# Kernel tuning notes

Hardware: AMD Instinct MI355X
Metric: run time of the kernel (lower is better)

Reference implementation:

```python
import jax, jax.numpy as jnp
import numpy as np


def setup_inputs() -> dict:
    key = jax.random.key(0)
    kq, kk, kv = jax.random.split(key, 3)
    B, L, S, H, E, D = 2, 2048, 2048, 16, 64, 64
    return {
        "queries": jax.random.normal(kq, (B, L, H, E), dtype=jnp.float32),
        "keys": jax.random.normal(kk, (B, S, H, E), dtype=jnp.float32),
        "values": jax.random.normal(kv, (B, S, H, D), dtype=jnp.float32),
    }


def reference(queries, keys, values):
    # FullAttention forward (mask_flag=False, dropout=0.0 -> identity)
    E = queries.shape[-1]
    scale = 1.0 / jnp.sqrt(jnp.asarray(E, dtype=queries.dtype))
    # scores: [B, H, L, S]
    scores = jnp.einsum('blhe,bshe->bhls', queries, keys)
    A = jax.nn.softmax(scale * scores, axis=-1)
    # output: [B, L, H, D]
    V = jnp.einsum('bhls,bshd->blhd', A, values)
    return V
```

## Files before the change

### kernel.cpp

```cpp
#include <hip/hip_runtime.h>
#include <hip/hip_bf16.h>
#include <string.h>


#define NB 2
#define LL 2048
#define SS 2048
#define HH 16
#define EE 64
#define DD 64
#define KVB 64
#define NT (SS / KVB)
#define NWG2 (NB * HH * (LL / 64))

typedef _Float16 f16x8 __attribute__((ext_vector_type(8)));
typedef float f32x4 __attribute__((ext_vector_type(4)));
typedef float f32x16 __attribute__((ext_vector_type(16)));
typedef unsigned uint2v __attribute__((ext_vector_type(2)));
typedef unsigned uint4v __attribute__((ext_vector_type(4)));
typedef const __attribute__((address_space(1))) void* gas_p;
typedef __attribute__((address_space(3))) void* las_p;

__device__ __forceinline__ unsigned pk2h(float a, float b) {
    auto h = __builtin_amdgcn_cvt_pkrtz(a, b);
    unsigned u;
    __builtin_memcpy(&u, &h, 4);
    return u;
}

__device__ __forceinline__ float fexp2(float x) {
#if defined(__has_builtin) && __has_builtin(__builtin_amdgcn_exp2f)
    return __builtin_amdgcn_exp2f(x);
#else
    return exp2f(x);
#endif
}

__device__ __forceinline__ void gll16(const void* g, void* l) {
    __builtin_amdgcn_global_load_lds((gas_p)g, (las_p)l, 16, 0, 0);
}

__device__ __forceinline__ uint2v plswap(unsigned a, unsigned b) {
#if defined(__has_builtin) && __has_builtin(__builtin_amdgcn_permlane32_swap)
    return __builtin_amdgcn_permlane32_swap(a, b, false, false);
#else
    unsigned ax = (unsigned)__shfl_xor((int)a, 32);
    unsigned bx = (unsigned)__shfl_xor((int)b, 32);
    int l32 = (int)(threadIdx.x & 32);
    uint2v r;
    r[0] = l32 ? bx : a;
    r[1] = l32 ? b : ax;
    return r;
#endif
}

__device__ __forceinline__ float fbits(unsigned u) {
    float f; __builtin_memcpy(&f, &u, 4); return f;
}
__device__ __forceinline__ unsigned ubits(float f) {
    unsigned u; __builtin_memcpy(&u, &f, 4); return u;
}
__device__ __forceinline__ float xmax32(float x) {
    uint2v r = plswap(ubits(x), ubits(x));
    return fmaxf(fbits(r[0]), fbits(r[1]));
}
__device__ __forceinline__ float xsum32(float x) {
    uint2v r = plswap(ubits(x), ubits(x));
    return fbits(r[0]) + fbits(r[1]);
}

__global__ __launch_bounds__(256) void prepKV(const float* __restrict__ K,
                                              const float* __restrict__ V,
                                              unsigned short* __restrict__ Kh,
                                              unsigned short* __restrict__ Vth) {
    const int NTILE = NB * HH * NT;
    const bool isV = blockIdx.x >= NTILE;
    const int tile = blockIdx.x & (NTILE - 1);
    const int it = tile & (NT - 1);
    const int bh = tile >> 5;
    const int b = bh >> 4, h = bh & 15;
    const int t = threadIdx.x;

    if (!isV) {
        const int s = t >> 2, ec = t & 3;
        const float* src = K + (((size_t)b * SS + it * KVB + s) * HH + h) * EE + ec * 16;
        f32x4 x0 = ((const f32x4*)src)[0];
        f32x4 x1 = ((const f32x4*)src)[1];
        f32x4 x2 = ((const f32x4*)src)[2];
        f32x4 x3 = ((const f32x4*)src)[3];
        uint4v c0, c1;
        c0.x = pk2h(x0[0], x0[1]); c0.y = pk2h(x0[2], x0[3]);
        c0.z = pk2h(x1[0], x1[1]); c0.w = pk2h(x1[2], x1[3]);
        c1.x = pk2h(x2[0], x2[1]); c1.y = pk2h(x2[2], x2[3]);
        c1.z = pk2h(x3[0], x3[1]); c1.w = pk2h(x3[2], x3[3]);
        char* dst = (char*)Kh + (size_t)tile * 8192;
        const int sw = (s & 7) << 4;
        *(uint4v*)(dst + ((s * 128 + ec * 32) ^ sw)) = c0;
        *(uint4v*)(dst + ((s * 128 + ec * 32 + 16) ^ sw)) = c1;
    } else {
        __shared__ float Vt[64 * 68];
        {
            const int s = t >> 2, dc = t & 3;
            const float* src = V + (((size_t)b * SS + it * KVB + s) * HH + h) * DD + dc * 16;
            f32x4 x0 = ((const f32x4*)src)[0];
            f32x4 x1 = ((const f32x4*)src)[1];
            f32x4 x2 = ((const f32x4*)src)[2];
            f32x4 x3 = ((const f32x4*)src)[3];
            float* row = Vt + s * 68 + dc * 16;
            ((f32x4*)row)[0] = x0; ((f32x4*)row)[1] = x1;
            ((f32x4*)row)[2] = x2; ((f32x4*)row)[3] = x3;
        }
        __syncthreads();
        {
            const int d = t >> 2, sc = t & 3;
            float w[16];
#pragma unroll
            for (int j = 0; j < 16; ++j) w[j] = Vt[(sc * 16 + j) * 68 + d];
            uint4v c0, c1;
            c0.x = pk2h(w[0], w[1]); c0.y = pk2h(w[2], w[3]);
            c0.z = pk2h(w[4], w[5]); c0.w = pk2h(w[6], w[7]);
            c1.x = pk2h(w[8], w[9]); c1.y = pk2h(w[10], w[11]);
            c1.z = pk2h(w[12], w[13]); c1.w = pk2h(w[14], w[15]);
            char* dst = (char*)Vth + (size_t)tile * 8192;
            const int sw = (d & 7) << 4;
            *(uint4v*)(dst + ((d * 128 + sc * 32) ^ sw)) = c0;
            *(uint4v*)(dst + ((d * 128 + sc * 32 + 16) ^ sw)) = c1;
        }
    }
}

__global__ __launch_bounds__(256, 4) void fattn4(const unsigned short* __restrict__ Kh,
                                                 const unsigned short* __restrict__ Vth,
                                                 const float* __restrict__ Q,
                                                 float* __restrict__ O) {
    __shared__ __align__(16) char LB[32768];
    __shared__ float msh[4][32];
    __shared__ float lsh[4][32];
    char* K0s = LB;
    char* K1s = LB + 8192;
    char* V0s = LB + 16384;
    char* V1s = LB + 24576;

    const int tid = threadIdx.x;
    const int lane = tid & 63;
    const int wid = tid >> 6;
    const int ln = lane & 31;
    const int hi = lane >> 5;
    const int qg = wid >> 1;
    const int sh = wid & 1;

    const int bid0 = blockIdx.x;
    const int bid = (bid0 & 7) * (NWG2 >> 3) + (bid0 >> 3);
    const int bh = bid >> 5;
    const int qt = bid & 31;
    const int b = bh >> 4, h = bh & 15;
    const int qrow = qt * 64 + qg * 32 + ln;

    const float qs = 0.125f * 1.44269504088896340736f;
    const float* qptr = Q + (((size_t)b * LL + qrow) * HH + h) * EE + hi * 8;
    f16x8 qf[4];
#pragma unroll
    for (int ks = 0; ks < 4; ++ks) {
        f32x4 a0 = *(const f32x4*)(qptr + ks * 16);
        f32x4 a1 = *(const f32x4*)(qptr + ks * 16 + 4);
        union { f16x8 v; unsigned u[4]; } cv;
        cv.u[0] = pk2h(a0[0] * qs, a0[1] * qs);
        cv.u[1] = pk2h(a0[2] * qs, a0[3] * qs);
        cv.u[2] = pk2h(a1[0] * qs, a1[1] * qs);
        cv.u[3] = pk2h(a1[2] * qs, a1[3] * qs);
        qf[ks] = cv.v;
    }

    f32x16 o0, o1;
#pragma unroll
    for (int i = 0; i < 16; ++i) { o0[i] = 0.f; o1[i] = 0.f; }
    float m = -1e30f, l = 0.f;

    const char* Kg = (const char*)Kh + (size_t)bh * (NT * 8192);
    const char* Vg = (const char*)Vth + (size_t)bh * (NT * 8192);

    auto STAGE = [&](int it, char* Ks, char* Vs) {
        const size_t off = (size_t)it * 8192 + wid * 2048 + lane * 16;
        gll16(Kg + off, Ks + wid * 2048);
        gll16(Kg + off + 1024, Ks + wid * 2048 + 1024);
        gll16(Vg + off, Vs + wid * 2048);
        gll16(Vg + off + 1024, Vs + wid * 2048 + 1024);
    };

    const int swz = (ln & 7) << 4;
    const int srow = sh * 32 + ln;
    const int vcol = sh * 64;

    auto COMPUTE = [&](const char* Ks, const char* Vs) {
        f32x16 st;
#pragma unroll
        for (int i = 0; i < 16; ++i) st[i] = 0.f;
        __builtin_amdgcn_s_setprio(1);
#pragma unroll
        for (int ks = 0; ks < 4; ++ks) {
            f16x8 kf = *(const f16x8*)(Ks + ((srow * 128 + ks * 32 + hi * 16) ^ swz));
            st = __builtin_amdgcn_mfma_f32_32x32x16_f16(kf, qf[ks], st, 0, 0, 0);
        }
        __builtin_amdgcn_s_setprio(0);

        float x0 = st[0], x1 = st[1], x2 = st[2], x3 = st[3];
#pragma unroll
        for (int r = 4; r < 16; r += 4) {
            x0 = fmaxf(x0, st[r]);
            x1 = fmaxf(x1, st[r + 1]);
            x2 = fmaxf(x2, st[r + 2]);
            x3 = fmaxf(x3, st[r + 3]);
        }
        float pmax = xmax32(fmaxf(fmaxf(x0, x1), fmaxf(x2, x3)));
        if (!__all(pmax - m <= 8.0f)) {
            const float mn = fmaxf(m, pmax);
            const float al = fexp2(m - mn);
            l *= al; m = mn;
#pragma unroll
            for (int i = 0; i < 16; ++i) { o0[i] *= al; o1[i] *= al; }
        }
        float t0 = 0.f, t1 = 0.f, t2 = 0.f, t3 = 0.f;
#pragma unroll
        for (int r = 0; r < 16; r += 4) {
            st[r] = fexp2(st[r] - m);
            st[r + 1] = fexp2(st[r + 1] - m);
            st[r + 2] = fexp2(st[r + 2] - m);
            st[r + 3] = fexp2(st[r + 3] - m);
            t0 += st[r]; t1 += st[r + 1]; t2 += st[r + 2]; t3 += st[r + 3];
        }
        l += (t0 + t1) + (t2 + t3);

        {
            uint2v r0 = plswap(pk2h(st[0], st[1]), pk2h(st[4], st[5]));
            uint2v r1 = plswap(pk2h(st[2], st[3]), pk2h(st[6], st[7]));
            union { f16x8 v; unsigned u[4]; } w;
            w.u[0] = r0[0]; w.u[1] = r1[0]; w.u[2] = r0[1]; w.u[3] = r1[1];
            f16x8 v0 = *(const f16x8*)(Vs + ((ln * 128 + vcol + hi * 16) ^ swz));
            f16x8 v1 = *(const f16x8*)(Vs + (((32 + ln) * 128 + vcol + hi * 16) ^ swz));
            __builtin_amdgcn_s_setprio(1);
            o0 = __builtin_amdgcn_mfma_f32_32x32x16_f16(v0, w.v, o0, 0, 0, 0);
            o1 = __builtin_amdgcn_mfma_f32_32x32x16_f16(v1, w.v, o1, 0, 0, 0);
            __builtin_amdgcn_s_setprio(0);
        }
        {
            uint2v r2 = plswap(pk2h(st[8], st[9]), pk2h(st[12], st[13]));
            uint2v r3 = plswap(pk2h(st[10], st[11]), pk2h(st[14], st[15]));
            union { f16x8 v; unsigned u[4]; } w;
            w.u[0] = r2[0]; w.u[1] = r3[0]; w.u[2] = r2[1]; w.u[3] = r3[1];
            f16x8 v0 = *(const f16x8*)(Vs + ((ln * 128 + vcol + 32 + hi * 16) ^ swz));
            f16x8 v1 = *(const f16x8*)(Vs + (((32 + ln) * 128 + vcol + 32 + hi * 16) ^ swz));
            __builtin_amdgcn_s_setprio(1);
            o0 = __builtin_amdgcn_mfma_f32_32x32x16_f16(v0, w.v, o0, 0, 0, 0);
            o1 = __builtin_amdgcn_mfma_f32_32x32x16_f16(v1, w.v, o1, 0, 0, 0);
            __builtin_amdgcn_s_setprio(0);
        }
    };

    STAGE(0, K0s, V0s);
    __syncthreads();
    for (int it = 0; it < NT; it += 2) {
        if (it + 1 < NT) STAGE(it + 1, K1s, V1s);
        COMPUTE(K0s, V0s);
        __syncthreads();
        if (it + 2 < NT) STAGE(it + 2, K0s, V0s);
        COMPUTE(K1s, V1s);
        __syncthreads();
    }

    l = xsum32(l);
    if (hi == 0) { msh[wid][ln] = m; lsh[wid][ln] = l; }
    __syncthreads();
    const float mo = msh[wid ^ 1][ln];
    const float lo = lsh[wid ^ 1][ln];
    const float ms = fmaxf(m, mo);
    const float f = fexp2(m - ms);
    const float fo = fexp2(mo - ms);
    const float lstar = l * f + lo * fo;

    float* pbuf = (float*)LB + qg * (32 * 65);
    if (sh == 1) {
#pragma unroll
        for (int r = 0; r < 16; ++r) {
            const int d = (r & 3) + 8 * (r >> 2) + 4 * hi;
            pbuf[ln * 65 + d] = o0[r] * f;
            pbuf[ln * 65 + 32 + d] = o1[r] * f;
        }
    }
    __syncthreads();
    if (sh == 0) {
        const float invl = 1.f / lstar;
        float* optr = O + (((size_t)b * LL + qrow) * HH + h) * DD;
#pragma unroll
        for (int t = 0; t < 4; ++t) {
            f32x4 w0, w1;
#pragma unroll
            for (int i = 0; i < 4; ++i) {
                const int d = t * 8 + hi * 4 + i;
                w0[i] = (o0[4 * t + i] * f + pbuf[ln * 65 + d]) * invl;
                w1[i] = (o1[4 * t + i] * f + pbuf[ln * 65 + 32 + d]) * invl;
            }
            *(f32x4*)(optr + t * 8 + hi * 4) = w0;
            *(f32x4*)(optr + 32 + t * 8 + hi * 4) = w1;
        }
    }
}

typedef unsigned u2f __attribute__((ext_vector_type(2)));
__global__ __launch_bounds__(256) void fattn1(const float* __restrict__ Q,
                                              const float* __restrict__ K,
                                              const float* __restrict__ V,
                                              float* __restrict__ O) {
    __shared__ __align__(16) short Klds[KVB * 64];
    __shared__ __align__(16) short Vtlds[64 * KVB];
    __shared__ __align__(16) short Plds[4][16 * 64];

    const int tid = threadIdx.x;
    const int lane = tid & 63;
    const int wid = tid >> 6;
    const int g = (lane >> 4) & 3;
    const int c = lane & 15;

    const int bid = blockIdx.x;
    const int bh = bid >> 5;
    const int qt = bid & 31;
    const int b = bh >> 4;
    const int h = bh & 15;
    const int q0 = qt * 64;

    const int qrow = q0 + wid * 16 + c;
    const float* qptr = Q + (((size_t)b * LL + qrow) * HH + h) * EE;
    const float qs = 0.125f * 1.44269504088896340736f;
    f16x8 qf[2];
#pragma unroll
    for (int kk = 0; kk < 2; ++kk) {
        f32x4 a0 = *(const f32x4*)(qptr + kk * 32 + g * 8);
        f32x4 a1 = *(const f32x4*)(qptr + kk * 32 + g * 8 + 4);
        union { f16x8 v; unsigned u[4]; } cv;
        cv.u[0] = pk2h(a0[0] * qs, a0[1] * qs);
        cv.u[1] = pk2h(a0[2] * qs, a0[3] * qs);
        cv.u[2] = pk2h(a1[0] * qs, a1[1] * qs);
        cv.u[3] = pk2h(a1[2] * qs, a1[3] * qs);
        qf[kk] = cv.v;
    }

    f32x4 osacc[4];
    const f32x4 fzero = {0.f, 0.f, 0.f, 0.f};
#pragma unroll
    for (int i = 0; i < 4; ++i) osacc[i] = fzero;
    float m_run = -1e30f;
    float l_run = 0.f;

    const int km = tid & 15;
    const int kr = tid >> 4;

    for (int it = 0; it < NT; ++it) {
        const int s_glob = it * KVB;
        f32x4 kreg[4];
#pragma unroll
        for (int p = 0; p < 4; ++p) {
            int s = kr + p * 16;
            kreg[p] = *(const f32x4*)(K + (((size_t)b * SS + s_glob + s) * HH + h) * EE + km * 4);
        }
        f32x4 vreg[4];
#pragma unroll
        for (int p = 0; p < 4; ++p) {
            int s = kr * 4 + p;
            vreg[p] = *(const f32x4*)(V + (((size_t)b * SS + s_glob + s) * HH + h) * DD + km * 4);
        }
        __syncthreads();
#pragma unroll
        for (int p = 0; p < 4; ++p) {
            int s = kr + p * 16;
            u2f w;
            w.x = pk2h(kreg[p][0], kreg[p][1]);
            w.y = pk2h(kreg[p][2], kreg[p][3]);
            int byte = (s * 128 + km * 8) ^ ((s & 7) << 4);
            *(u2f*)((char*)Klds + byte) = w;
        }
#pragma unroll
        for (int i = 0; i < 4; ++i) {
            int d = km * 4 + i;
            u2f w;
            w.x = pk2h(vreg[0][i], vreg[1][i]);
            w.y = pk2h(vreg[2][i], vreg[3][i]);
            int byte = (d * 128 + kr * 8) ^ ((d & 7) << 4);
            *(u2f*)((char*)Vtlds + byte) = w;
        }
        __syncthreads();

        f32x4 stv[4];
#pragma unroll
        for (int fr = 0; fr < 4; ++fr) stv[fr] = fzero;
#pragma unroll
        for (int fr = 0; fr < 4; ++fr) {
            int s = fr * 16 + c;
            f16x8 kf0 = *(const f16x8*)((const char*)Klds + ((s * 128 + 16 * g) ^ ((s & 7) << 4)));
            stv[fr] = __builtin_amdgcn_mfma_f32_16x16x32_f16(kf0, qf[0], stv[fr], 0, 0, 0);
            f16x8 kf1 = *(const f16x8*)((const char*)Klds + ((s * 128 + 64 + 16 * g) ^ ((s & 7) << 4)));
            stv[fr] = __builtin_amdgcn_mfma_f32_16x16x32_f16(kf1, qf[1], stv[fr], 0, 0, 0);
        }

        float pmax = stv[0][0];
#pragma unroll
        for (int fr = 0; fr < 4; ++fr)
#pragma unroll
            for (int r = 0; r < 4; ++r) pmax = fmaxf(pmax, stv[fr][r]);
        pmax = fmaxf(pmax, __shfl_xor(pmax, 16));
        pmax = fmaxf(pmax, __shfl_xor(pmax, 32));
        float mnew = fmaxf(m_run, pmax);
        float alpha = fexp2(m_run - mnew);
        float tsum = 0.f;
#pragma unroll
        for (int fr = 0; fr < 4; ++fr)
#pragma unroll
            for (int r = 0; r < 4; ++r) {
                float e = fexp2(stv[fr][r] - mnew);
                stv[fr][r] = e;
                tsum += e;
            }
        tsum += __shfl_xor(tsum, 16);
        tsum += __shfl_xor(tsum, 32);
        l_run = l_run * alpha + tsum;
        m_run = mnew;
#pragma unroll
        for (int fr = 0; fr < 4; ++fr)
#pragma unroll
            for (int r = 0; r < 4; ++r) osacc[fr][r] *= alpha;

        short* plb = &Plds[wid][0];
#pragma unroll
        for (int fr = 0; fr < 4; ++fr) {
            u2f w;
            w.x = pk2h(stv[fr][0], stv[fr][1]);
            w.y = pk2h(stv[fr][2], stv[fr][3]);
            int byte = (c * 128 + fr * 32 + g * 8) ^ ((c & 7) << 4);
            *(u2f*)((char*)plb + byte) = w;
        }
        f16x8 pb0 = *(const f16x8*)((const char*)plb + ((c * 128 + 16 * g) ^ ((c & 7) << 4)));
        f16x8 pb1 = *(const f16x8*)((const char*)plb + ((c * 128 + 64 + 16 * g) ^ ((c & 7) << 4)));

#pragma unroll
        for (int fr = 0; fr < 4; ++fr) {
            int d = fr * 16 + c;
            f16x8 vf0 = *(const f16x8*)((const char*)Vtlds + ((d * 128 + 16 * g) ^ ((d & 7) << 4)));
            osacc[fr] = __builtin_amdgcn_mfma_f32_16x16x32_f16(vf0, pb0, osacc[fr], 0, 0, 0);
            f16x8 vf1 = *(const f16x8*)((const char*)Vtlds + ((d * 128 + 64 + 16 * g) ^ ((d & 7) << 4)));
            osacc[fr] = __builtin_amdgcn_mfma_f32_16x16x32_f16(vf1, pb1, osacc[fr], 0, 0, 0);
        }
    }

    float invl = 1.f / l_run;
    float* optr = O + (((size_t)b * LL + qrow) * HH + h) * DD;
#pragma unroll
    for (int fr = 0; fr < 4; ++fr) {
        f32x4 o;
        o[0] = osacc[fr][0] * invl;
        o[1] = osacc[fr][1] * invl;
        o[2] = osacc[fr][2] * invl;
        o[3] = osacc[fr][3] * invl;
        *(f32x4*)(optr + fr * 16 + g * 4) = o;
    }
}

extern "C" void kernel_launch(void* const* d_in, const int* in_sizes, int n_in,
                              void* d_out, int out_size, void* d_ws, size_t ws_size,
                              hipStream_t stream) {
    const float* Q = (const float*)d_in[0];
    const float* K = (const float*)d_in[1];
    const float* V = (const float*)d_in[2];
    float* Op = (float*)d_out;

    const size_t halfBytes = (size_t)NB * HH * SS * EE * 2;
    if (ws_size >= 2 * halfBytes) {
        unsigned short* Kht = (unsigned short*)d_ws;
        unsigned short* Vht = (unsigned short*)((char*)d_ws + halfBytes);
        hipLaunchKernelGGL(prepKV, dim3(2 * NB * HH * NT), dim3(256), 0, stream, K, V, Kht, Vht);
        hipLaunchKernelGGL(fattn4, dim3(NWG2), dim3(256), 0, stream, Kht, Vht, Q, Op);
    } else {
        hipLaunchKernelGGL(fattn1, dim3(NB * HH * (LL / 64)), dim3(256), 0, stream, Q, K, V, Op);
    }
}
```

Before: 67.48 us.

## Load V fragments directly from global and software-pipeline QK with softmax-PV

Stops staging V tiles through LDS: each lane now reads its V fragments straight from global memory into registers, and only K is double-buffered in LDS, which shrinks shared memory from about 33KB to about 18KB. The loop is restructured so the QK MFMA for the next tile is issued before the softmax and PV of the current tile, overlapping matrix work with exp and reduction work. The trade is uncoalesced global V loads with their latency exposed inside the loop, plus extra registers for a second score accumulator.

```diff
diff --git a/kernel.cpp b/kernel.cpp
--- a/kernel.cpp
+++ b/kernel.cpp
@@ -129,17 +129,11 @@
     }
 }
 
-__global__ __launch_bounds__(256, 4) void fattn4(const unsigned short* __restrict__ Kh,
+__global__ __launch_bounds__(256, 4) void fattn5(const unsigned short* __restrict__ Kh,
                                                  const unsigned short* __restrict__ Vth,
                                                  const float* __restrict__ Q,
                                                  float* __restrict__ O) {
-    __shared__ __align__(16) char LB[32768];
-    __shared__ float msh[4][32];
-    __shared__ float lsh[4][32];
-    char* K0s = LB;
-    char* K1s = LB + 8192;
-    char* V0s = LB + 16384;
-    char* V1s = LB + 24576;
+    __shared__ __align__(16) char LB[18176];
 
     const int tid = threadIdx.x;
     const int lane = tid & 63;
@@ -155,6 +149,9 @@
     const int qt = bid & 31;
     const int b = bh >> 4, h = bh & 15;
     const int qrow = qt * 64 + qg * 32 + ln;
+
+    char* KA = LB;
+    char* KB = LB + 8192;
 
     const float qs = 0.125f * 1.44269504088896340736f;
     const float* qptr = Q + (((size_t)b * LL + qrow) * HH + h) * EE + hi * 8;
@@ -179,20 +176,21 @@
     const char* Kg = (const char*)Kh + (size_t)bh * (NT * 8192);
     const char* Vg = (const char*)Vth + (size_t)bh * (NT * 8192);
 
-    auto STAGE = [&](int it, char* Ks, char* Vs) {
+    const int swz = (ln & 7) << 4;
+    const int srow = sh * 32 + ln;
+    const int vcol = sh * 64;
+    const int vo00 = (ln * 128 + vcol + hi * 16) ^ swz;
+    const int vo01 = ((32 + ln) * 128 + vcol + hi * 16) ^ swz;
+    const int vo10 = (ln * 128 + vcol + 32 + hi * 16) ^ swz;
+    const int vo11 = ((32 + ln) * 128 + vcol + 32 + hi * 16) ^ swz;
+
+    auto STAGE_K = [&](int it, char* Ks) {
         const size_t off = (size_t)it * 8192 + wid * 2048 + lane * 16;
         gll16(Kg + off, Ks + wid * 2048);
         gll16(Kg + off + 1024, Ks + wid * 2048 + 1024);
-        gll16(Vg + off, Vs + wid * 2048);
-        gll16(Vg + off + 1024, Vs + wid * 2048 + 1024);
     };
 
-    const int swz = (ln & 7) << 4;
-    const int srow = sh * 32 + ln;
-    const int vcol = sh * 64;
-
-    auto COMPUTE = [&](const char* Ks, const char* Vs) {
-        f32x16 st;
+    auto QK = [&](const char* Ks, f32x16& st) {
 #pragma unroll
         for (int i = 0; i < 16; ++i) st[i] = 0.f;
         __builtin_amdgcn_s_setprio(1);
@@ -202,7 +200,9 @@
             st = __builtin_amdgcn_mfma_f32_32x32x16_f16(kf, qf[ks], st, 0, 0, 0);
         }
         __builtin_amdgcn_s_setprio(0);
-
+    };
+
+    auto SMPV = [&](f32x16& st, f16x8 v00, f16x8 v01, f16x8 v10, f16x8 v11) {
         float x0 = st[0], x1 = st[1], x2 = st[2], x3 = st[3];
 #pragma unroll
         for (int r = 4; r < 16; r += 4) {
@@ -235,11 +235,9 @@
             uint2v r1 = plswap(pk2h(st[2], st[3]), pk2h(st[6], st[7]));
             union { f16x8 v; unsigned u[4]; } w;
             w.u[0] = r0[0]; w.u[1] = r1[0]; w.u[2] = r0[1]; w.u[3] = r1[1];
-            f16x8 v0 = *(const f16x8*)(Vs + ((ln * 128 + vcol + hi * 16) ^ swz));
-            f16x8 v1 = *(const f16x8*)(Vs + (((32 + ln) * 128 + vcol + hi * 16) ^ swz));
             __builtin_amdgcn_s_setprio(1);
-            o0 = __builtin_amdgcn_mfma_f32_32x32x16_f16(v0, w.v, o0, 0, 0, 0);
-            o1 = __builtin_amdgcn_mfma_f32_32x32x16_f16(v1, w.v, o1, 0, 0, 0);
+            o0 = __builtin_amdgcn_mfma_f32_32x32x16_f16(v00, w.v, o0, 0, 0, 0);
+            o1 = __builtin_amdgcn_mfma_f32_32x32x16_f16(v01, w.v, o1, 0, 0, 0);
             __builtin_amdgcn_s_setprio(0);
         }
         {
@@ -247,31 +245,48 @@
             uint2v r3 = plswap(pk2h(st[10], st[11]), pk2h(st[14], st[15]));
             union { f16x8 v; unsigned u[4]; } w;
             w.u[0] = r2[0]; w.u[1] = r3[0]; w.u[2] = r2[1]; w.u[3] = r3[1];
-            f16x8 v0 = *(const f16x8*)(Vs + ((ln * 128 + vcol + 32 + hi * 16) ^ swz));
-            f16x8 v1 = *(const f16x8*)(Vs + (((32 + ln) * 128 + vcol + 32 + hi * 16) ^ swz));
             __builtin_amdgcn_s_setprio(1);
-            o0 = __builtin_amdgcn_mfma_f32_32x32x16_f16(v0, w.v, o0, 0, 0, 0);
-            o1 = __builtin_amdgcn_mfma_f32_32x32x16_f16(v1, w.v, o1, 0, 0, 0);
+            o0 = __builtin_amdgcn_mfma_f32_32x32x16_f16(v10, w.v, o0, 0, 0, 0);
+            o1 = __builtin_amdgcn_mfma_f32_32x32x16_f16(v11, w.v, o1, 0, 0, 0);
             __builtin_amdgcn_s_setprio(0);
         }
     };
 
-    STAGE(0, K0s, V0s);
+    f32x16 stA, stB;
+    STAGE_K(0, KA);
     __syncthreads();
-    for (int it = 0; it < NT; it += 2) {
-        if (it + 1 < NT) STAGE(it + 1, K1s, V1s);
-        COMPUTE(K0s, V0s);
+    STAGE_K(1, KB);
+    QK(KA, stA);
+
+    for (int t = 0; t < NT; t += 2) {
         __syncthreads();
-        if (it + 2 < NT) STAGE(it + 2, K0s, V0s);
-        COMPUTE(K1s, V1s);
+        if (t + 2 < NT) STAGE_K(t + 2, KA);
+        const char* vt0 = Vg + (size_t)t * 8192;
+        f16x8 v00 = *(const f16x8*)(vt0 + vo00);
+        f16x8 v01 = *(const f16x8*)(vt0 + vo01);
+        f16x8 v10 = *(const f16x8*)(vt0 + vo10);
+        f16x8 v11 = *(const f16x8*)(vt0 + vo11);
+        if (t + 1 < NT) QK(KB, stB);
+        SMPV(stA, v00, v01, v10, v11);
+
         __syncthreads();
-    }
-
+        if (t + 3 < NT) STAGE_K(t + 3, KB);
+        const char* vt1 = Vg + (size_t)(t + 1) * 8192;
+        f16x8 w00 = *(const f16x8*)(vt1 + vo00);
+        f16x8 w01 = *(const f16x8*)(vt1 + vo01);
+        f16x8 w10 = *(const f16x8*)(vt1 + vo10);
+        f16x8 w11 = *(const f16x8*)(vt1 + vo11);
+        if (t + 2 < NT) QK(KA, stA);
+        SMPV(stB, w00, w01, w10, w11);
+    }
+
+    float* msh = (float*)(LB + 16896);
+    float* lsh = (float*)(LB + 17408);
     l = xsum32(l);
-    if (hi == 0) { msh[wid][ln] = m; lsh[wid][ln] = l; }
+    if (hi == 0) { msh[wid * 32 + ln] = m; lsh[wid * 32 + ln] = l; }
     __syncthreads();
-    const float mo = msh[wid ^ 1][ln];
-    const float lo = lsh[wid ^ 1][ln];
+    const float mo = msh[(wid ^ 1) * 32 + ln];
+    const float lo = lsh[(wid ^ 1) * 32 + ln];
     const float ms = fmaxf(m, mo);
     const float f = fexp2(m - ms);
     const float fo = fexp2(mo - ms);
@@ -434,7 +449,7 @@
             w.x = pk2h(stv[fr][0], stv[fr][1]);
             w.y = pk2h(stv[fr][2], stv[fr][3]);
             int byte = (c * 128 + fr * 32 + g * 8) ^ ((c & 7) << 4);
-            *(u2f*)((char*)plb + byte) = w;
+            *(u2f*)((char*)Plds + (wid * 4096 + byte)) = w;
         }
         f16x8 pb0 = *(const f16x8*)((const char*)plb + ((c * 128 + 16 * g) ^ ((c & 7) << 4)));
         f16x8 pb1 = *(const f16x8*)((const char*)plb + ((c * 128 + 64 + 16 * g) ^ ((c & 7) << 4)));
@@ -475,7 +490,7 @@
         unsigned short* Kht = (unsigned short*)d_ws;
         unsigned short* Vht = (unsigned short*)((char*)d_ws + halfBytes);
         hipLaunchKernelGGL(prepKV, dim3(2 * NB * HH * NT), dim3(256), 0, stream, K, V, Kht, Vht);
-        hipLaunchKernelGGL(fattn4, dim3(NWG2), dim3(256), 0, stream, Kht, Vht, Q, Op);
+        hipLaunchKernelGGL(fattn5, dim3(NWG2), dim3(256), 0, stream, Kht, Vht, Q, Op);
     } else {
         hipLaunchKernelGGL(fattn1, dim3(NB * HH * (LL / 64)), dim3(256), 0, stream, Q, K, V, Op);
     }
```

New measurement: 95.71 us. 41.8% more time.
